# Optimization experiments

Measured on AMD Instinct MI355X. Metric: run time of the kernel, lower is better.

The kernel has to match this reference:

```python
import jax, jax.numpy as jnp
import numpy as np

# model hyperparameters (from init_kwargs 'model' mapping)
SIG = 10.0       # kernel length scale
C = 0.0          # energy integration constant
STD = 1.0        # normalization std
M, N_ATOMS = 64, 24
T_ROWS, DESC = 6000, N_ATOMS * (N_ATOMS - 1) // 2  # 276


def setup_inputs() -> dict:
    key = jax.random.key(0)
    k1, k2, k3 = jax.random.split(key, 3)
    # spread atoms out so pairwise distances are O(1..10) Angstrom-like
    Rs = jax.random.normal(k1, (M, N_ATOMS, 3), jnp.float32) * 3.0
    # training descriptors are inverse distances -> positive values in (0,1)
    xs_train = jax.random.uniform(k2, (T_ROWS, DESC), jnp.float32)
    Jx_alphas = jax.random.normal(k3, (T_ROWS, DESC), jnp.float32) * 0.1
    return {"Rs": Rs, "xs_train": xs_train, "Jx_alphas": Jx_alphas}


def reference(Rs, xs_train, Jx_alphas):
    sig = SIG
    q = np.sqrt(5.0) / sig
    m, n = Rs.shape[0], Rs.shape[1]
    i, j = np.tril_indices(n, k=-1)  # lower-triangular atom pairs, P entries

    # pairwise coordinate differences [M, N, N, 3]
    diffs = Rs[:, :, None, :] - Rs[:, None, :, :]
    # inverse pairwise distances over tril pairs -> descriptor xs [M, P]
    d_ij = jnp.linalg.norm(diffs[:, i, j, :], axis=-1)
    xs = 1.0 / d_ij

    # descriptor differences to all (permuted) training points [M, T, P]
    x_diffs = q * xs[:, None, :] - q * xs_train[None, :, :]
    x_dists = jnp.linalg.norm(x_diffs, axis=-1)            # [M, T]
    exp_xs = (5.0 / (3.0 * sig ** 2)) * jnp.exp(-x_dists)  # [M, T]
    dot = jnp.einsum('mtp,tp->mt', x_diffs, Jx_alphas)     # [M, T]
    exp1 = exp_xs * (1.0 + x_dists)                        # [M, T]

    F1 = jnp.einsum('mt,mtp->mp', exp_xs * dot, x_diffs)   # [M, P]
    F2 = exp1 @ Jx_alphas                                  # [M, P]
    Fs_x = (F1 - F2) * xs ** 3                             # [M, P]

    # scatter pair forces back onto the symmetric [N, N] pair grid;
    # diagonal diffs are zero so leaving mult=0 there matches the original
    mult = jnp.zeros((m, n, n), Rs.dtype)
    mult = mult.at[:, i, j].set(Fs_x).at[:, j, i].set(Fs_x)
    Fs = (diffs * mult[..., None]).sum(axis=1) * STD       # [M, N, 3]

    Es = (exp1 * dot).sum(axis=-1) / q * STD + C           # [M]
    return Es, Fs
```

## Files before the change

kernel.cpp:

```cpp
#include <hip/hip_runtime.h>
#include <math.h>

#define MM 64
#define NA 24
#define NP 276
#define NT 6000
#define QC 0.22360679774997896f
#define EXPC 0.01666666666666667f

#define G2S   56
#define G2R   108

#define OFF_WT   0
#define OFF_ET   387072
#define OFF_SLAB 774144
#define OFF_ESP  2752512
#define OFF_SWP  2776512
#define OFF_XS2  2800512
#define OFF_UU   2818176
#define OFF_VV   2818240
#define OFF_C1   2824240
#define OFF_F    2830240
#define SLABSTRIDE 35328

__device__ __forceinline__ void p2ij(int p, int& i, int& j) {
  int ii = (int)((1.0f + sqrtf(1.0f + 8.0f * (float)p)) * 0.5f);
  while (ii * (ii - 1) / 2 > p) ii--;
  while ((ii + 1) * ii / 2 <= p) ii++;
  j = p - ii * (ii - 1) / 2;
  i = ii;
}

__global__ __launch_bounds__(256) void k_pre(const float* __restrict__ Rs,
                                             const float* __restrict__ xt,
                                             const float* __restrict__ Ja,
                                             float* __restrict__ ws) {
  const int tid = threadIdx.x;
  const int bid = blockIdx.x;
  if (bid < MM) {
    if (bid < 2) {
      float* tz = ws + (bid ? OFF_ET : OFF_WT) + (size_t)NT * 64;
      for (int z = tid; z < 48 * 64; z += 256) tz[z] = 0.f;
    }
    const int m = bid;
    __shared__ float sR[NA * 3];
    __shared__ float sAcc[4];
    if (tid < NA * 3) sR[tid] = Rs[m * NA * 3 + tid];
    __syncthreads();
    float acc = 0.f;
    for (int p = tid; p < NP; p += 256) {
      int i, j;
      p2ij(p, i, j);
      const float dx = sR[i * 3 + 0] - sR[j * 3 + 0];
      const float dy = sR[i * 3 + 1] - sR[j * 3 + 1];
      const float dz = sR[i * 3 + 2] - sR[j * 3 + 2];
      const float u = 1.0f / sqrtf(dx * dx + dy * dy + dz * dz);
      ws[OFF_XS2 + (size_t)(m >> 5) * NP * 32 + p * 32 + (m & 31)] = u;
      acc = fmaf(u, u, acc);
    }
#pragma unroll
    for (int off = 32; off; off >>= 1) acc += __shfl_down(acc, off);
    if ((tid & 63) == 0) sAcc[tid >> 6] = acc;
    __syncthreads();
    if (tid == 0) ws[OFF_UU + m] = sAcc[0] + sAcc[1] + sAcc[2] + sAcc[3];
  } else {
    const int sb = bid - MM;
    const int t = sb * 4 + (tid >> 6);
    const int lane = tid & 63;
    const float* xr = xt + (size_t)t * NP;
    const float* jr = Ja + (size_t)t * NP;
    float a = 0.f, b = 0.f;
#pragma unroll
    for (int q = 0; q < 4; q++) {
      const float v = xr[lane + 64 * q];
      const float jj = jr[lane + 64 * q];
      a = fmaf(v, v, a);
      b = fmaf(v, jj, b);
    }
    if (lane < NP - 256) {
      const float v = xr[256 + lane];
      const float jj = jr[256 + lane];
      a = fmaf(v, v, a);
      b = fmaf(v, jj, b);
    }
#pragma unroll
    for (int off = 32; off; off >>= 1) {
      a += __shfl_down(a, off);
      b += __shfl_down(b, off);
    }
    if (lane == 0) { ws[OFF_VV + t] = a; ws[OFF_C1 + t] = b; }
  }
}

#define K1SUB(A, vb0, vb1, jb0, jb1)                                               \
  av0[0] = fmaf(A.x, vb0, av0[0]); av0[1] = fmaf(A.y, vb0, av0[1]);                \
  av0[2] = fmaf(A.z, vb0, av0[2]); av0[3] = fmaf(A.w, vb0, av0[3]);                \
  av1[0] = fmaf(A.x, vb1, av1[0]); av1[1] = fmaf(A.y, vb1, av1[1]);                \
  av1[2] = fmaf(A.z, vb1, av1[2]); av1[3] = fmaf(A.w, vb1, av1[3]);                \
  aj0[0] = fmaf(A.x, jb0, aj0[0]); aj0[1] = fmaf(A.y, jb0, aj0[1]);                \
  aj0[2] = fmaf(A.z, jb0, aj0[2]); aj0[3] = fmaf(A.w, jb0, aj0[3]);                \
  aj1[0] = fmaf(A.x, jb1, aj1[0]); aj1[1] = fmaf(A.y, jb1, aj1[1]);                \
  aj1[2] = fmaf(A.z, jb1, aj1[2]); aj1[3] = fmaf(A.w, jb1, aj1[3]);

__global__ __launch_bounds__(256, 2) void k1(const float* __restrict__ xt,
                                             const float* __restrict__ Ja,
                                             float* __restrict__ ws) {
  __shared__ __align__(16) float Bv[16 * NP];
  __shared__ __align__(16) float Bj[16 * NP];
  __shared__ __align__(16) float As[NP * 32];
  const int tid = threadIdx.x;
  const int t0 = blockIdx.x * 16;
  const int m0 = blockIdx.y * 32;
  const int w = tid >> 6;
  const int lane = tid & 63;
  const int mg = lane & 7;
  const int tg = lane >> 3;

  const float4 uu4 = *(const float4*)(ws + OFF_UU + m0 + 4 * mg);
  const float2 vv2 = *(const float2*)(ws + OFF_VV + t0 + 2 * tg);
  const float2 c12 = *(const float2*)(ws + OFF_C1 + t0 + 2 * tg);

  {
    const float4* xs4 = (const float4*)(xt + (size_t)t0 * NP);
    const float4* js4 = (const float4*)(Ja + (size_t)t0 * NP);
    const float4* as4 = (const float4*)(ws + OFF_XS2 + (size_t)blockIdx.y * NP * 32);
    float4* bv4 = (float4*)Bv;
    float4* bj4 = (float4*)Bj;
    float4* a4  = (float4*)As;
    for (int i = tid; i < 16 * NP / 4; i += 256) { bv4[i] = xs4[i]; bj4[i] = js4[i]; }
    for (int i = tid; i < NP * 32 / 4; i += 256) a4[i] = as4[i];
  }
  __syncthreads();

  float av0[4] = {0.f, 0.f, 0.f, 0.f}, av1[4] = {0.f, 0.f, 0.f, 0.f};
  float aj0[4] = {0.f, 0.f, 0.f, 0.f}, aj1[4] = {0.f, 0.f, 0.f, 0.f};
  const float* BvR0 = Bv + (2 * tg + 0) * NP;
  const float* BvR1 = Bv + (2 * tg + 1) * NP;
  const float* BjR0 = Bj + (2 * tg + 0) * NP;
  const float* BjR1 = Bj + (2 * tg + 1) * NP;
  const float* Ac = As + 4 * mg;
  const int kbeg = w * 68;
  const int kend = (w == 3) ? NP : (kbeg + 68);
#pragma unroll 2
  for (int k = kbeg; k < kend; k += 4) {
    const float4 a0 = *(const float4*)(Ac + (k + 0) * 32);
    const float4 a1 = *(const float4*)(Ac + (k + 1) * 32);
    const float4 a2 = *(const float4*)(Ac + (k + 2) * 32);
    const float4 a3 = *(const float4*)(Ac + (k + 3) * 32);
    const float4 bv0 = *(const float4*)(BvR0 + k);
    const float4 bv1 = *(const float4*)(BvR1 + k);
    const float4 bj0 = *(const float4*)(BjR0 + k);
    const float4 bj1 = *(const float4*)(BjR1 + k);
    K1SUB(a0, bv0.x, bv1.x, bj0.x, bj1.x)
    K1SUB(a1, bv0.y, bv1.y, bj0.y, bj1.y)
    K1SUB(a2, bv0.z, bv1.z, bj0.z, bj1.z)
    K1SUB(a3, bv0.w, bv1.w, bj0.w, bj1.w)
  }
  __syncthreads();

  if (w > 0) {
    float* red = As + (size_t)(w - 1) * 16 * 64;
#pragma unroll
    for (int q = 0; q < 4; q++) {
      red[(q + 0) * 64 + lane]  = av0[q];
      red[(q + 4) * 64 + lane]  = av1[q];
      red[(q + 8) * 64 + lane]  = aj0[q];
      red[(q + 12) * 64 + lane] = aj1[q];
    }
  }
  __syncthreads();
  if (w == 0) {
#pragma unroll
    for (int ww = 0; ww < 3; ww++) {
      const float* red = As + (size_t)ww * 16 * 64;
#pragma unroll
      for (int q = 0; q < 4; q++) {
        av0[q] += red[(q + 0) * 64 + lane];
        av1[q] += red[(q + 4) * 64 + lane];
        aj0[q] += red[(q + 8) * 64 + lane];
        aj1[q] += red[(q + 12) * 64 + lane];
      }
    }
    float es[4] = {0.f, 0.f, 0.f, 0.f}, swv[4] = {0.f, 0.f, 0.f, 0.f};
    const float uum[4] = {uu4.x, uu4.y, uu4.z, uu4.w};
#pragma unroll
    for (int tj = 0; tj < 2; tj++) {
      const float vvt = tj ? vv2.y : vv2.x;
      const float c1t = tj ? c12.y : c12.x;
      const float* g1 = tj ? av1 : av0;
      const float* g2 = tj ? aj1 : aj0;
      float wq[4], eq[4];
#pragma unroll
      for (int mi = 0; mi < 4; mi++) {
        const float d2 = fmaxf(uum[mi] - 2.f * g1[mi] + vvt, 0.f);
        const float xd = QC * sqrtf(d2);
        const float dv = QC * (g2[mi] - c1t);
        const float ex = EXPC * __expf(-xd);
        const float e1v = ex * (1.f + xd);
        const float w_ = ex * dv;
        wq[mi] = w_; eq[mi] = e1v;
        es[mi] += e1v * dv; swv[mi] += w_;
      }
      const int t = t0 + 2 * tg + tj;
      *(float4*)(ws + OFF_WT + (size_t)t * 64 + m0 + 4 * mg) = make_float4(wq[0], wq[1], wq[2], wq[3]);
      *(float4*)(ws + OFF_ET + (size_t)t * 64 + m0 + 4 * mg) = make_float4(eq[0], eq[1], eq[2], eq[3]);
    }
#pragma unroll
    for (int q = 0; q < 4; q++) {
      es[q] += __shfl_down(es[q], 32); es[q] += __shfl_down(es[q], 16); es[q] += __shfl_down(es[q], 8);
      swv[q] += __shfl_down(swv[q], 32); swv[q] += __shfl_down(swv[q], 16); swv[q] += __shfl_down(swv[q], 8);
    }
    if (lane < 8) {
      *(float4*)(ws + OFF_ESP + (size_t)blockIdx.x * 64 + m0 + 4 * lane) =
          make_float4(es[0], es[1], es[2], es[3]);
      *(float4*)(ws + OFF_SWP + (size_t)blockIdx.x * 64 + m0 + 4 * lane) =
          make_float4(swv[0], swv[1], swv[2], swv[3]);
    }
  }
}

__global__ __launch_bounds__(256, 2) void k2(const float* __restrict__ xt,
                                             const float* __restrict__ Ja,
                                             float* __restrict__ ws) {
  __shared__ __align__(16) float Aw[G2R * 64];
  __shared__ __align__(16) float Ae[G2R * 64];
  __shared__ __align__(16) float2 Bvj[G2R][16];
  const int tid = threadIdx.x;
  const int p0 = blockIdx.x * 16;
  const int cid = blockIdx.y;
  const int k0 = cid * G2R;
  const int validp = (NP - p0 < 16) ? (NP - p0) : 16;
  const int w = tid >> 6;
  const int lane = tid & 63;
  const int mg = lane & 15;
  const int pg = lane >> 4;

  {
    const float4* aws = (const float4*)(ws + OFF_WT + (size_t)k0 * 64);
    const float4* aes = (const float4*)(ws + OFF_ET + (size_t)k0 * 64);
    float4* aw4 = (float4*)Aw;
    float4* ae4 = (float4*)Ae;
    for (int idx = tid; idx < G2R * 16; idx += 256) { aw4[idx] = aws[idx]; ae4[idx] = aes[idx]; }
  }
  for (int idx = tid; idx < G2R * 4; idx += 256) {
    const int k = idx >> 2;
    const int pq = (idx & 3) * 4;
    const int t = k0 + k;
    float4 v = make_float4(0.f, 0.f, 0.f, 0.f), j = v;
    if (pq < validp && t < NT) {
      v = *(const float4*)(xt + (size_t)t * NP + p0 + pq);
      j = *(const float4*)(Ja + (size_t)t * NP + p0 + pq);
    }
    *(float4*)&Bvj[k][pq]     = make_float4(v.x, j.x, v.y, j.y);
    *(float4*)&Bvj[k][pq + 2] = make_float4(v.z, j.z, v.w, j.w);
  }
  __syncthreads();

  float f1[4][4] = {{0.f}}, f2[4][4] = {{0.f}};
  const float* AwL = Aw + 4 * mg;
  const float* AeL = Ae + 4 * mg;
  const int kb = w * 27;
  const int ke = kb + 27;
#pragma unroll 3
  for (int k = kb; k < ke; ++k) {
    const float4 aw = *(const float4*)(AwL + (size_t)k * 64);
    const float4 ae = *(const float4*)(AeL + (size_t)k * 64);
    const float4 b01 = *(const float4*)&Bvj[k][4 * pg];
    const float4 b23 = *(const float4*)&Bvj[k][4 * pg + 2];
    const float vb[4] = {b01.x, b01.z, b23.x, b23.z};
    const float jb[4] = {b01.y, b01.w, b23.y, b23.w};
    const float aww[4] = {aw.x, aw.y, aw.z, aw.w};
    const float aee[4] = {ae.x, ae.y, ae.z, ae.w};
#pragma unroll
    for (int mi = 0; mi < 4; mi++)
#pragma unroll
      for (int pj = 0; pj < 4; pj++) {
        f1[mi][pj] = fmaf(aww[mi], vb[pj], f1[mi][pj]);
        f2[mi][pj] = fmaf(aee[mi], jb[pj], f2[mi][pj]);
      }
  }
  __syncthreads();

  if (w > 0) {
    float* red = Aw + (size_t)(w - 1) * 32 * 64;
#pragma unroll
    for (int mi = 0; mi < 4; mi++)
#pragma unroll
      for (int pj = 0; pj < 4; pj++) {
        red[(mi * 4 + pj) * 64 + lane]        = f1[mi][pj];
        red[(16 + mi * 4 + pj) * 64 + lane]   = f2[mi][pj];
      }
  }
  __syncthreads();
  if (w == 0) {
#pragma unroll
    for (int ww = 0; ww < 3; ww++) {
      const float* red = Aw + (size_t)ww * 32 * 64;
#pragma unroll
      for (int mi = 0; mi < 4; mi++)
#pragma unroll
        for (int pj = 0; pj < 4; pj++) {
          f1[mi][pj] += red[(mi * 4 + pj) * 64 + lane];
          f2[mi][pj] += red[(16 + mi * 4 + pj) * 64 + lane];
        }
    }
    float* b1 = ws + OFF_SLAB + (size_t)(cid * 2 + 0) * NP * 64;
    float* b2 = ws + OFF_SLAB + (size_t)(cid * 2 + 1) * NP * 64;
#pragma unroll
    for (int pj = 0; pj < 4; pj++) {
      const int pl = 4 * pg + pj;
      if (pl < validp) {
        const int p = p0 + pl;
        *(float4*)(b1 + (size_t)p * 64 + 4 * mg) =
            make_float4(f1[0][pj], f1[1][pj], f1[2][pj], f1[3][pj]);
        *(float4*)(b2 + (size_t)p * 64 + 4 * mg) =
            make_float4(f2[0][pj], f2[1][pj], f2[2][pj], f2[3][pj]);
      }
    }
  }
}

__global__ __launch_bounds__(128) void k_red(float* __restrict__ ws) {
  const int inner = blockIdx.x * 128 + threadIdx.x;
  const float* src = ws + OFF_SLAB + inner;
  float s = 0.f;
#pragma unroll
  for (int cid = 0; cid < G2S; cid++) s += src[(size_t)cid * SLABSTRIDE];
  ws[OFF_F + inner] = s;
}

__global__ __launch_bounds__(320) void k3(const float* __restrict__ Rs,
                                          const float* __restrict__ ws,
                                          float* __restrict__ out) {
  const int m = blockIdx.x;
  const int tid = threadIdx.x;
  __shared__ float fx[NP];
  __shared__ float sR[NA * 3];
  __shared__ float sEsw[5], sSww[5];
  __shared__ float sTot[2];
  if (tid < NA * 3) sR[tid] = Rs[m * NA * 3 + tid];

  float aE = 0.f, aS = 0.f;
  for (int tt = tid; tt < 375; tt += 320) {
    aE += ws[OFF_ESP + (size_t)tt * 64 + m];
    aS += ws[OFF_SWP + (size_t)tt * 64 + m];
  }
#pragma unroll
  for (int off = 32; off; off >>= 1) {
    aE += __shfl_down(aE, off);
    aS += __shfl_down(aS, off);
  }
  if ((tid & 63) == 0) { sEsw[tid >> 6] = aE; sSww[tid >> 6] = aS; }
  __syncthreads();
  if (tid == 0) {
    float e = 0.f, s = 0.f;
#pragma unroll
    for (int w = 0; w < 5; w++) { e += sEsw[w]; s += sSww[w]; }
    sTot[0] = e; sTot[1] = s;
    out[m] = e / QC;
  }
  __syncthreads();
  const float sw = sTot[1];

  for (int p = tid; p < NP; p += 320) {
    const float f1p = ws[OFF_F + (size_t)0 * NP * 64 + p * 64 + m];
    const float f2  = ws[OFF_F + (size_t)1 * NP * 64 + p * 64 + m];
    const float u = ws[OFF_XS2 + (size_t)(m >> 5) * NP * 32 + p * 32 + (m & 31)];
    const float F1 = QC * (u * sw - f1p);
    fx[p] = (F1 - f2) * u * u * u;
  }
  __syncthreads();

  if (tid < NA * 3) {
    const int a = tid / 3, cc = tid % 3;
    const float ra = sR[a * 3 + cc];
    float acc = 0.f;
    for (int b = 0; b < NA; b++) {
      if (b == a) continue;
      const int i = a > b ? a : b, j = a > b ? b : a;
      const int p = i * (i - 1) / 2 + j;
      acc += (sR[b * 3 + cc] - ra) * fx[p];
    }
    out[MM + m * NA * 3 + tid] = acc;
  }
}

extern "C" void kernel_launch(void* const* d_in, const int* in_sizes, int n_in,
                              void* d_out, int out_size, void* d_ws, size_t ws_size,
                              hipStream_t stream) {
  const float* Rs = (const float*)d_in[0];
  const float* xt = (const float*)d_in[1];
  const float* Ja = (const float*)d_in[2];
  float* out = (float*)d_out;
  float* ws = (float*)d_ws;

  k_pre<<<MM + 1500, 256, 0, stream>>>(Rs, xt, Ja, ws);
  k1<<<dim3(375, 2), 256, 0, stream>>>(xt, Ja, ws);
  k2<<<dim3(18, G2S), 256, 0, stream>>>(xt, Ja, ws);
  k_red<<<NP * 2, 128, 0, stream>>>(ws);
  k3<<<MM, 320, 0, stream>>>(Rs, ws, out);
}
```

Baseline: 115.3 us.

## Fold per-row norms into k1, double k2 split-K blocks, widen reduction

```diff
diff --git a/kernel.cpp b/kernel.cpp
--- a/kernel.cpp
+++ b/kernel.cpp
@@ -8,19 +8,17 @@
 #define QC 0.22360679774997896f
 #define EXPC 0.01666666666666667f
 
-#define G2S   56
-#define G2R   108
+#define G2S   112
+#define G2R   54
 
 #define OFF_WT   0
 #define OFF_ET   387072
 #define OFF_SLAB 774144
-#define OFF_ESP  2752512
-#define OFF_SWP  2776512
-#define OFF_XS2  2800512
-#define OFF_UU   2818176
-#define OFF_VV   2818240
-#define OFF_C1   2824240
-#define OFF_F    2830240
+#define OFF_ESP  4730880
+#define OFF_SWP  4754880
+#define OFF_XS2  4778880
+#define OFF_UU   4796544
+#define OFF_F    4796608
 #define SLABSTRIDE 35328
 
 __device__ __forceinline__ void p2ij(int p, int& i, int& j) {
@@ -32,64 +30,33 @@
 }
 
 __global__ __launch_bounds__(256) void k_pre(const float* __restrict__ Rs,
-                                             const float* __restrict__ xt,
-                                             const float* __restrict__ Ja,
                                              float* __restrict__ ws) {
   const int tid = threadIdx.x;
-  const int bid = blockIdx.x;
-  if (bid < MM) {
-    if (bid < 2) {
-      float* tz = ws + (bid ? OFF_ET : OFF_WT) + (size_t)NT * 64;
-      for (int z = tid; z < 48 * 64; z += 256) tz[z] = 0.f;
-    }
-    const int m = bid;
-    __shared__ float sR[NA * 3];
-    __shared__ float sAcc[4];
-    if (tid < NA * 3) sR[tid] = Rs[m * NA * 3 + tid];
-    __syncthreads();
-    float acc = 0.f;
-    for (int p = tid; p < NP; p += 256) {
-      int i, j;
-      p2ij(p, i, j);
-      const float dx = sR[i * 3 + 0] - sR[j * 3 + 0];
-      const float dy = sR[i * 3 + 1] - sR[j * 3 + 1];
-      const float dz = sR[i * 3 + 2] - sR[j * 3 + 2];
-      const float u = 1.0f / sqrtf(dx * dx + dy * dy + dz * dz);
-      ws[OFF_XS2 + (size_t)(m >> 5) * NP * 32 + p * 32 + (m & 31)] = u;
-      acc = fmaf(u, u, acc);
-    }
-#pragma unroll
-    for (int off = 32; off; off >>= 1) acc += __shfl_down(acc, off);
-    if ((tid & 63) == 0) sAcc[tid >> 6] = acc;
-    __syncthreads();
-    if (tid == 0) ws[OFF_UU + m] = sAcc[0] + sAcc[1] + sAcc[2] + sAcc[3];
-  } else {
-    const int sb = bid - MM;
-    const int t = sb * 4 + (tid >> 6);
-    const int lane = tid & 63;
-    const float* xr = xt + (size_t)t * NP;
-    const float* jr = Ja + (size_t)t * NP;
-    float a = 0.f, b = 0.f;
-#pragma unroll
-    for (int q = 0; q < 4; q++) {
-      const float v = xr[lane + 64 * q];
-      const float jj = jr[lane + 64 * q];
-      a = fmaf(v, v, a);
-      b = fmaf(v, jj, b);
-    }
-    if (lane < NP - 256) {
-      const float v = xr[256 + lane];
-      const float jj = jr[256 + lane];
-      a = fmaf(v, v, a);
-      b = fmaf(v, jj, b);
-    }
-#pragma unroll
-    for (int off = 32; off; off >>= 1) {
-      a += __shfl_down(a, off);
-      b += __shfl_down(b, off);
-    }
-    if (lane == 0) { ws[OFF_VV + t] = a; ws[OFF_C1 + t] = b; }
-  }
+  const int m = blockIdx.x;
+  if (m < 2) {
+    float* tz = ws + (m ? OFF_ET : OFF_WT) + (size_t)NT * 64;
+    for (int z = tid; z < 48 * 64; z += 256) tz[z] = 0.f;
+  }
+  __shared__ float sR[NA * 3];
+  __shared__ float sAcc[4];
+  if (tid < NA * 3) sR[tid] = Rs[m * NA * 3 + tid];
+  __syncthreads();
+  float acc = 0.f;
+  for (int p = tid; p < NP; p += 256) {
+    int i, j;
+    p2ij(p, i, j);
+    const float dx = sR[i * 3 + 0] - sR[j * 3 + 0];
+    const float dy = sR[i * 3 + 1] - sR[j * 3 + 1];
+    const float dz = sR[i * 3 + 2] - sR[j * 3 + 2];
+    const float u = 1.0f / sqrtf(dx * dx + dy * dy + dz * dz);
+    ws[OFF_XS2 + (size_t)(m >> 5) * NP * 32 + p * 32 + (m & 31)] = u;
+    acc = fmaf(u, u, acc);
+  }
+#pragma unroll
+  for (int off = 32; off; off >>= 1) acc += __shfl_down(acc, off);
+  if ((tid & 63) == 0) sAcc[tid >> 6] = acc;
+  __syncthreads();
+  if (tid == 0) ws[OFF_UU + m] = sAcc[0] + sAcc[1] + sAcc[2] + sAcc[3];
 }
 
 #define K1SUB(A, vb0, vb1, jb0, jb1)                                               \
@@ -108,6 +75,7 @@
   __shared__ __align__(16) float Bv[16 * NP];
   __shared__ __align__(16) float Bj[16 * NP];
   __shared__ __align__(16) float As[NP * 32];
+  __shared__ float sVV[16], sC1[16];
   const int tid = threadIdx.x;
   const int t0 = blockIdx.x * 16;
   const int m0 = blockIdx.y * 32;
@@ -117,8 +85,6 @@
   const int tg = lane >> 3;
 
   const float4 uu4 = *(const float4*)(ws + OFF_UU + m0 + 4 * mg);
-  const float2 vv2 = *(const float2*)(ws + OFF_VV + t0 + 2 * tg);
-  const float2 c12 = *(const float2*)(ws + OFF_C1 + t0 + 2 * tg);
 
   {
     const float4* xs4 = (const float4*)(xt + (size_t)t0 * NP);
@@ -131,6 +97,25 @@
     for (int i = tid; i < NP * 32 / 4; i += 256) a4[i] = as4[i];
   }
   __syncthreads();
+
+  {
+    const int tl = tid >> 4;
+    const int l16 = tid & 15;
+    const float* bvr = Bv + tl * NP;
+    const float* bjr = Bj + tl * NP;
+    float a = 0.f, b = 0.f;
+    for (int k = l16; k < NP; k += 16) {
+      const float v = bvr[k];
+      a = fmaf(v, v, a);
+      b = fmaf(v, bjr[k], b);
+    }
+#pragma unroll
+    for (int off = 8; off; off >>= 1) {
+      a += __shfl_down(a, off, 16);
+      b += __shfl_down(b, off, 16);
+    }
+    if (l16 == 0) { sVV[tl] = a; sC1[tl] = b; }
+  }
 
   float av0[4] = {0.f, 0.f, 0.f, 0.f}, av1[4] = {0.f, 0.f, 0.f, 0.f};
   float aj0[4] = {0.f, 0.f, 0.f, 0.f}, aj1[4] = {0.f, 0.f, 0.f, 0.f};
@@ -185,8 +170,8 @@
     const float uum[4] = {uu4.x, uu4.y, uu4.z, uu4.w};
 #pragma unroll
     for (int tj = 0; tj < 2; tj++) {
-      const float vvt = tj ? vv2.y : vv2.x;
-      const float c1t = tj ? c12.y : c12.x;
+      const float vvt = sVV[2 * tg + tj];
+      const float c1t = sC1[2 * tg + tj];
       const float* g1 = tj ? av1 : av0;
       const float* g2 = tj ? aj1 : aj0;
       float wq[4], eq[4];
@@ -219,12 +204,13 @@
   }
 }
 
-__global__ __launch_bounds__(256, 2) void k2(const float* __restrict__ xt,
+__global__ __launch_bounds__(256, 4) void k2(const float* __restrict__ xt,
                                              const float* __restrict__ Ja,
                                              float* __restrict__ ws) {
-  __shared__ __align__(16) float Aw[G2R * 64];
-  __shared__ __align__(16) float Ae[G2R * 64];
-  __shared__ __align__(16) float2 Bvj[G2R][16];
+  __shared__ __align__(16) float S[G2R * 64 * 2 + G2R * 32];
+  float* Aw = S;
+  float* Ae = S + G2R * 64;
+  float2* Bvj = (float2*)(S + 2 * G2R * 64);
   const int tid = threadIdx.x;
   const int p0 = blockIdx.x * 16;
   const int cid = blockIdx.y;
@@ -242,31 +228,31 @@
     float4* ae4 = (float4*)Ae;
     for (int idx = tid; idx < G2R * 16; idx += 256) { aw4[idx] = aws[idx]; ae4[idx] = aes[idx]; }
   }
-  for (int idx = tid; idx < G2R * 4; idx += 256) {
-    const int k = idx >> 2;
-    const int pq = (idx & 3) * 4;
+  if (tid < G2R * 4) {
+    const int k = tid >> 2;
+    const int pq = (tid & 3) * 4;
     const int t = k0 + k;
     float4 v = make_float4(0.f, 0.f, 0.f, 0.f), j = v;
     if (pq < validp && t < NT) {
       v = *(const float4*)(xt + (size_t)t * NP + p0 + pq);
       j = *(const float4*)(Ja + (size_t)t * NP + p0 + pq);
     }
-    *(float4*)&Bvj[k][pq]     = make_float4(v.x, j.x, v.y, j.y);
-    *(float4*)&Bvj[k][pq + 2] = make_float4(v.z, j.z, v.w, j.w);
+    *(float4*)&Bvj[k * 16 + pq]     = make_float4(v.x, j.x, v.y, j.y);
+    *(float4*)&Bvj[k * 16 + pq + 2] = make_float4(v.z, j.z, v.w, j.w);
   }
   __syncthreads();
 
   float f1[4][4] = {{0.f}}, f2[4][4] = {{0.f}};
   const float* AwL = Aw + 4 * mg;
   const float* AeL = Ae + 4 * mg;
-  const int kb = w * 27;
-  const int ke = kb + 27;
-#pragma unroll 3
+  const int kb = (w * G2R) >> 2;
+  const int ke = ((w + 1) * G2R) >> 2;
+#pragma unroll 2
   for (int k = kb; k < ke; ++k) {
     const float4 aw = *(const float4*)(AwL + (size_t)k * 64);
     const float4 ae = *(const float4*)(AeL + (size_t)k * 64);
-    const float4 b01 = *(const float4*)&Bvj[k][4 * pg];
-    const float4 b23 = *(const float4*)&Bvj[k][4 * pg + 2];
+    const float4 b01 = *(const float4*)&Bvj[k * 16 + 4 * pg];
+    const float4 b23 = *(const float4*)&Bvj[k * 16 + 4 * pg + 2];
     const float vb[4] = {b01.x, b01.z, b23.x, b23.z};
     const float jb[4] = {b01.y, b01.w, b23.y, b23.w};
     const float aww[4] = {aw.x, aw.y, aw.z, aw.w};
@@ -282,20 +268,20 @@
   __syncthreads();
 
   if (w > 0) {
-    float* red = Aw + (size_t)(w - 1) * 32 * 64;
+    float* red = S + (size_t)(w - 1) * 2048;
 #pragma unroll
     for (int mi = 0; mi < 4; mi++)
 #pragma unroll
       for (int pj = 0; pj < 4; pj++) {
-        red[(mi * 4 + pj) * 64 + lane]        = f1[mi][pj];
-        red[(16 + mi * 4 + pj) * 64 + lane]   = f2[mi][pj];
+        red[(mi * 4 + pj) * 64 + lane]      = f1[mi][pj];
+        red[(16 + mi * 4 + pj) * 64 + lane] = f2[mi][pj];
       }
   }
   __syncthreads();
   if (w == 0) {
 #pragma unroll
     for (int ww = 0; ww < 3; ww++) {
-      const float* red = Aw + (size_t)ww * 32 * 64;
+      const float* red = S + (size_t)ww * 2048;
 #pragma unroll
       for (int mi = 0; mi < 4; mi++)
 #pragma unroll
@@ -320,11 +306,11 @@
   }
 }
 
-__global__ __launch_bounds__(128) void k_red(float* __restrict__ ws) {
-  const int inner = blockIdx.x * 128 + threadIdx.x;
+__global__ __launch_bounds__(256) void k_red(float* __restrict__ ws) {
+  const int inner = blockIdx.x * 256 + threadIdx.x;
   const float* src = ws + OFF_SLAB + inner;
   float s = 0.f;
-#pragma unroll
+#pragma unroll 4
   for (int cid = 0; cid < G2S; cid++) s += src[(size_t)cid * SLABSTRIDE];
   ws[OFF_F + inner] = s;
 }
@@ -394,9 +380,9 @@
   float* out = (float*)d_out;
   float* ws = (float*)d_ws;
 
-  k_pre<<<MM + 1500, 256, 0, stream>>>(Rs, xt, Ja, ws);
+  k_pre<<<MM, 256, 0, stream>>>(Rs, ws);
   k1<<<dim3(375, 2), 256, 0, stream>>>(xt, Ja, ws);
   k2<<<dim3(18, G2S), 256, 0, stream>>>(xt, Ja, ws);
-  k_red<<<NP * 2, 128, 0, stream>>>(ws);
+  k_red<<<138, 256, 0, stream>>>(ws);
   k3<<<MM, 320, 0, stream>>>(Rs, ws, out);
 }
```

Result: slower. 124.6 us (+8.1%).
